# Kernel optimization log

Hardware: AMD Instinct MI355X
Metric: run time of the kernel (lower is better)

## Reference

```python
import jax, jax.numpy as jnp
import numpy as np

N = 20000      # tuple-graph nodes
E = 320000     # edges per relation
F_IN = 5189    # 80 one-hot + 3*1703 node features
DIM = 256
N_ORIG = 183   # original texas graph nodes
C = 7


def _gcn(x, W, b, src, dst, n):
    # PyG GCNConv: add self loops, symmetric deg^-1/2 normalization, aggregate src->dst.
    loop = jnp.arange(n)
    s = jnp.concatenate([src, loop])
    d = jnp.concatenate([dst, loop])
    deg = jax.ops.segment_sum(jnp.ones(s.shape[0], x.dtype), d, num_segments=n)
    dinv = jnp.where(deg > 0, jax.lax.rsqrt(deg), 0.0)
    norm = dinv[s] * dinv[d]            # [E+n]
    h = x @ W                            # [n, dim]
    out = jax.ops.segment_sum(h[s] * norm[:, None], d, num_segments=n)
    return out + b


def _mlp(h, w1, b1, w2, b2):
    return jnp.maximum(h @ w1 + b1, 0.0) @ w2 + b2


def _seg_mean(h, idx, n):
    s = jax.ops.segment_sum(h, idx, num_segments=n)
    cnt = jax.ops.segment_sum(jnp.ones(idx.shape[0], h.dtype), idx, num_segments=n)
    return s / jnp.maximum(cnt, 1.0)[:, None]


def setup_inputs() -> dict:
    key = jax.random.key(0)
    ks = jax.random.split(key, 16)
    sc_in = 1.0 / np.sqrt(F_IN)
    sc_d = 1.0 / np.sqrt(DIM)
    sc_3d = 1.0 / np.sqrt(3 * DIM)
    inp = {
        'x': jax.random.normal(ks[0], (N, F_IN), jnp.float32),
        'w1': jax.random.normal(ks[1], (3, F_IN, DIM), jnp.float32) * sc_in,
        'b1': jnp.zeros((3, DIM), jnp.float32),
        'w2': jax.random.normal(ks[2], (3, DIM, DIM), jnp.float32) * sc_d,
        'b2': jnp.zeros((3, DIM), jnp.float32),
        'm1w1': jax.random.normal(ks[3], (3 * DIM, DIM), jnp.float32) * sc_3d,
        'm1b1': jnp.zeros((DIM,), jnp.float32),
        'm1w2': jax.random.normal(ks[4], (DIM, DIM), jnp.float32) * sc_d,
        'm1b2': jnp.zeros((DIM,), jnp.float32),
        'm2w1': jax.random.normal(ks[5], (3 * DIM, DIM), jnp.float32) * sc_3d,
        'm2b1': jnp.zeros((DIM,), jnp.float32),
        'm2w2': jax.random.normal(ks[6], (DIM, DIM), jnp.float32) * sc_d,
        'm2b2': jnp.zeros((DIM,), jnp.float32),
        'mw1': jax.random.normal(ks[7], (3 * DIM, DIM), jnp.float32) * sc_3d,
        'mb1': jnp.zeros((DIM,), jnp.float32),
        'mw2': jax.random.normal(ks[8], (DIM, C), jnp.float32) * sc_d,
        'mb2': jnp.zeros((C,), jnp.float32),
        'edge_index_1': jax.random.randint(ks[9], (2, E), 0, N),
        'edge_index_2': jax.random.randint(ks[10], (2, E), 0, N),
        'edge_index_3': jax.random.randint(ks[11], (2, E), 0, N),
        'index_1': jax.random.randint(ks[12], (N,), 0, N_ORIG),
        'index_2': jax.random.randint(ks[13], (N,), 0, N_ORIG),
        'index_3': jax.random.randint(ks[14], (N,), 0, N_ORIG),
    }
    return inp


def reference(x, w1, b1, w2, b2, m1w1, m1b1, m1w2, m1b2,
              m2w1, m2b1, m2w2, m2b2, mw1, mb1, mw2, mb2,
              edge_index_1, edge_index_2, edge_index_3,
              index_1, index_2, index_3):
    n = x.shape[0]
    eis = (edge_index_1, edge_index_2, edge_index_3)
    # layer 1: three GCN convs over the three relations, ReLU, concat, MLP
    hs = [jnp.maximum(_gcn(x, w1[i], b1[i], eis[i][0], eis[i][1], n), 0.0) for i in range(3)]
    h = _mlp(jnp.concatenate(hs, axis=-1), m1w1, m1b1, m1w2, m1b2)
    # layer 2
    hs = [jnp.maximum(_gcn(h, w2[i], b2[i], eis[i][0], eis[i][1], n), 0.0) for i in range(3)]
    h = _mlp(jnp.concatenate(hs, axis=-1), m2w1, m2b1, m2w2, m2b2)
    # faithful to source bug: index_2 is overwritten by index_3 before scatter
    x1 = _seg_mean(h, index_1, N_ORIG)
    x2 = _seg_mean(h, index_3, N_ORIG)
    x3 = _seg_mean(h, index_3, N_ORIG)
    out = _mlp(jnp.concatenate([x1, x2, x3], axis=1), mw1, mb1, mw2, mb2)
    return jax.nn.log_softmax(out, axis=1)
```

## Files before the change

kernel.cpp:

```cpp
#include <hip/hip_runtime.h>
#include <hip/hip_bf16.h>
#include <cstdint>
#include <cstddef>

typedef __bf16 bf16_t;
typedef __bf16 bf16x8 __attribute__((ext_vector_type(8)));
typedef __bf16 bf16x4 __attribute__((ext_vector_type(4)));
typedef float f32x4 __attribute__((ext_vector_type(4)));

#define NN 20000
#define NE 320000
#define FIN 5189
#define KP1 5216
#define NORIG 183

__device__ inline f32x4 ld4u(const float* p) {
  f32x4 v; __builtin_memcpy(&v, p, 16); return v;
}

__device__ inline void gload_lds16(const bf16_t* g, bf16_t* l) {
  __builtin_amdgcn_global_load_lds(
      (const __attribute__((address_space(1))) uint32_t*)g,
      (__attribute__((address_space(3))) uint32_t*)l, 16, 0, 0);
}

__device__ inline int swz(int r) { return (r ^ (r >> 2)) & 3; }

__global__ void k_cvtpad(const float* __restrict__ x, bf16_t* __restrict__ xb) {
  const int total = NN * (KP1 / 8);
  for (int idx = blockIdx.x * 256 + threadIdx.x; idx < total; idx += gridDim.x * 256) {
    int row = idx / (KP1 / 8);
    int c8  = idx - row * (KP1 / 8);
    int col = c8 * 8;
    bf16x8 v{};
    const float* xp = x + (size_t)row * FIN + col;
    if (col + 8 <= FIN) {
      f32x4 a = ld4u(xp), b = ld4u(xp + 4);
#pragma unroll
      for (int j = 0; j < 4; ++j) { v[j] = (bf16_t)a[j]; v[4 + j] = (bf16_t)b[j]; }
    } else {
#pragma unroll
      for (int j = 0; j < 8; ++j) v[j] = (col + j < FIN) ? (bf16_t)xp[j] : (bf16_t)0.f;
    }
    *(bf16x8*)&xb[(size_t)row * KP1 + col] = v;
  }
}

__global__ __launch_bounds__(512) void k_gemm_w(
    const bf16_t* __restrict__ A, const bf16_t* __restrict__ Bt,
    bf16_t* __restrict__ C, const float* __restrict__ bias,
    const float* __restrict__ dscale,
    int M, int N, int Kp, int relu, int NBX)
{
  __shared__ __align__(16) bf16_t As[2][128 * 32];
  __shared__ __align__(16) bf16_t Bs[2][256 * 32];
  const int nwg = gridDim.x;
  const int q = nwg >> 3, rr = nwg & 7;
  const int xcd = blockIdx.x & 7, jj = blockIdx.x >> 3;
  const int L = (xcd < rr ? xcd * (q + 1) : rr * (q + 1) + (xcd - rr) * q) + jj;
  const int bx = L % NBX, by = L / NBX;

  const int tid = threadIdx.x, lane = tid & 63, wave = tid >> 6;
  const int m0 = by * 128, n0 = bx * 256;
  const int wr = (wave >> 2) * 64, wc = (wave & 3) * 64;
  const int fm = lane & 15, fs = lane >> 4;

  const int arow = tid >> 2, asl = tid & 3;
  const int aks = asl ^ swz(arow);
  int agrow = m0 + arow; if (agrow >= M) agrow = M - 1;
  const bf16_t* asrc = A + (size_t)agrow * Kp + aks * 8;

  const int br0 = tid >> 2, br1 = 128 + br0;
  const bf16_t* bsrc0 = Bt + (size_t)(n0 + br0) * Kp + (asl ^ swz(br0)) * 8;
  const bf16_t* bsrc1 = Bt + (size_t)(n0 + br1) * Kp + (asl ^ swz(br1)) * 8;

  bf16_t* adst  = &As[0][0] + wave * 512;
  bf16_t* bdst0 = &Bs[0][0] + wave * 512;
  bf16_t* bdst1 = &Bs[0][0] + 4096 + wave * 512;

  int aoff[4], boff[4];
#pragma unroll
  for (int i = 0; i < 4; ++i) {
    int ra = wr + i * 16 + fm;
    aoff[i] = ra * 32 + (fs ^ swz(ra)) * 8;
    int rb = wc + i * 16 + fm;
    boff[i] = rb * 32 + (fs ^ swz(rb)) * 8;
  }

  f32x4 acc[4][4];
#pragma unroll
  for (int i = 0; i < 4; ++i)
#pragma unroll
    for (int j = 0; j < 4; ++j) acc[i][j] = {0.f, 0.f, 0.f, 0.f};

#define STAGEW(buf, kof) do { \
    gload_lds16(asrc + (kof),  adst  + (buf) * (128 * 32)); \
    gload_lds16(bsrc0 + (kof), bdst0 + (buf) * (256 * 32)); \
    gload_lds16(bsrc1 + (kof), bdst1 + (buf) * (256 * 32)); \
  } while (0)

  const int NT = Kp / 32;
  STAGEW(0, 0);
  __syncthreads();
  int buf = 0;
  for (int t = 0; t < NT - 1; ++t) {
    STAGEW(buf ^ 1, (t + 1) * 32);
    bf16x8 af[4], bfv[4];
#pragma unroll
    for (int i = 0; i < 4; ++i) af[i] = *(const bf16x8*)&As[buf][aoff[i]];
#pragma unroll
    for (int j = 0; j < 4; ++j) bfv[j] = *(const bf16x8*)&Bs[buf][boff[j]];
#pragma unroll
    for (int i = 0; i < 4; ++i)
#pragma unroll
      for (int j = 0; j < 4; ++j)
        acc[i][j] = __builtin_amdgcn_mfma_f32_16x16x32_bf16(af[i], bfv[j], acc[i][j], 0, 0, 0);
    __syncthreads();
    buf ^= 1;
  }
  {
    bf16x8 af[4], bfv[4];
#pragma unroll
    for (int i = 0; i < 4; ++i) af[i] = *(const bf16x8*)&As[buf][aoff[i]];
#pragma unroll
    for (int j = 0; j < 4; ++j) bfv[j] = *(const bf16x8*)&Bs[buf][boff[j]];
#pragma unroll
    for (int i = 0; i < 4; ++i)
#pragma unroll
      for (int j = 0; j < 4; ++j)
        acc[i][j] = __builtin_amdgcn_mfma_f32_16x16x32_bf16(af[i], bfv[j], acc[i][j], 0, 0, 0);
  }

  const int ccol = n0 + wc + fm;
  const int rrel = (n0 + wc) >> 8;
  const float* dsp = dscale ? dscale + (size_t)rrel * NN : nullptr;
#pragma unroll
  for (int i = 0; i < 4; ++i) {
    const int rb2 = m0 + wr + i * 16 + (lane >> 4) * 4;
#pragma unroll
    for (int r = 0; r < 4; ++r) {
      const int row = rb2 + r;
      if (row < M) {
        bf16_t* cp = C + (size_t)row * N + ccol;
        const float sc = dsp ? dsp[row] : 1.f;
#pragma unroll
        for (int j = 0; j < 4; ++j) {
          float v = acc[i][j][r];
          if (bias) v += bias[ccol + j * 16];
          if (relu) v = fmaxf(v, 0.f);
          cp[j * 16] = (bf16_t)(v * sc);
        }
      }
    }
  }
}

__global__ __launch_bounds__(256) void k_gemm_s(
    const bf16_t* __restrict__ A, const bf16_t* __restrict__ Bt,
    bf16_t* __restrict__ C, const float* __restrict__ bias,
    int M, int N, int Kp, int relu)
{
  __shared__ __align__(16) bf16_t As[2][128 * 32];
  __shared__ __align__(16) bf16_t Bs[2][128 * 32];
  const int tid = threadIdx.x, lane = tid & 63, wave = tid >> 6;
  const int m0 = blockIdx.y * 128, n0 = blockIdx.x * 128;
  const int wr = (wave >> 1) * 64, wc = (wave & 1) * 64;
  const int fm = lane & 15, fs = lane >> 4;

  const int r0 = tid >> 2, r1 = 64 + r0, sl = tid & 3;
  int ag0 = m0 + r0; if (ag0 >= M) ag0 = M - 1;
  int ag1 = m0 + r1; if (ag1 >= M) ag1 = M - 1;
  const bf16_t* asrc0 = A + (size_t)ag0 * Kp + (sl ^ swz(r0)) * 8;
  const bf16_t* asrc1 = A + (size_t)ag1 * Kp + (sl ^ swz(r1)) * 8;
  const bf16_t* bsrc0 = Bt + (size_t)(n0 + r0) * Kp + (sl ^ swz(r0)) * 8;
  const bf16_t* bsrc1 = Bt + (size_t)(n0 + r1) * Kp + (sl ^ swz(r1)) * 8;

  bf16_t* adst0 = &As[0][0] + wave * 512;
  bf16_t* adst1 = &As[0][0] + 2048 + wave * 512;
  bf16_t* bdst0 = &Bs[0][0] + wave * 512;
  bf16_t* bdst1 = &Bs[0][0] + 2048 + wave * 512;

  int aoff[4], boff[4];
#pragma unroll
  for (int i = 0; i < 4; ++i) {
    int ra = wr + i * 16 + fm;
    aoff[i] = ra * 32 + (fs ^ swz(ra)) * 8;
    int rb = wc + i * 16 + fm;
    boff[i] = rb * 32 + (fs ^ swz(rb)) * 8;
  }

  f32x4 acc[4][4];
#pragma unroll
  for (int i = 0; i < 4; ++i)
#pragma unroll
    for (int j = 0; j < 4; ++j) acc[i][j] = {0.f, 0.f, 0.f, 0.f};

#define STAGES(buf, kof) do { \
    gload_lds16(asrc0 + (kof), adst0 + (buf) * (128 * 32)); \
    gload_lds16(asrc1 + (kof), adst1 + (buf) * (128 * 32)); \
    gload_lds16(bsrc0 + (kof), bdst0 + (buf) * (128 * 32)); \
    gload_lds16(bsrc1 + (kof), bdst1 + (buf) * (128 * 32)); \
  } while (0)

  const int NT = Kp / 32;
  STAGES(0, 0);
  __syncthreads();
  int buf = 0;
  for (int t = 0; t < NT - 1; ++t) {
    STAGES(buf ^ 1, (t + 1) * 32);
    bf16x8 af[4], bfv[4];
#pragma unroll
    for (int i = 0; i < 4; ++i) af[i] = *(const bf16x8*)&As[buf][aoff[i]];
#pragma unroll
    for (int j = 0; j < 4; ++j) bfv[j] = *(const bf16x8*)&Bs[buf][boff[j]];
#pragma unroll
    for (int i = 0; i < 4; ++i)
#pragma unroll
      for (int j = 0; j < 4; ++j)
        acc[i][j] = __builtin_amdgcn_mfma_f32_16x16x32_bf16(af[i], bfv[j], acc[i][j], 0, 0, 0);
    __syncthreads();
    buf ^= 1;
  }
  {
    bf16x8 af[4], bfv[4];
#pragma unroll
    for (int i = 0; i < 4; ++i) af[i] = *(const bf16x8*)&As[buf][aoff[i]];
#pragma unroll
    for (int j = 0; j < 4; ++j) bfv[j] = *(const bf16x8*)&Bs[buf][boff[j]];
#pragma unroll
    for (int i = 0; i < 4; ++i)
#pragma unroll
      for (int j = 0; j < 4; ++j)
        acc[i][j] = __builtin_amdgcn_mfma_f32_16x16x32_bf16(af[i], bfv[j], acc[i][j], 0, 0, 0);
  }

  const int ccol = n0 + wc + fm;
#pragma unroll
  for (int i = 0; i < 4; ++i) {
    const int rb2 = m0 + wr + i * 16 + (lane >> 4) * 4;
#pragma unroll
    for (int r = 0; r < 4; ++r) {
      const int row = rb2 + r;
      if (row < M) {
        bf16_t* cp = C + (size_t)row * N + ccol;
#pragma unroll
        for (int j = 0; j < 4; ++j) {
          float v = acc[i][j][r];
          if (bias) v += bias[ccol + j * 16];
          if (relu) v = fmaxf(v, 0.f);
          cp[j * 16] = (bf16_t)v;
        }
      }
    }
  }
}

__global__ void k_transw(const float* __restrict__ src, bf16_t* __restrict__ dst,
                         int K, int Kp)
{
  __shared__ float tile[32][33];
  const int g = blockIdx.z;
  const int k0 = blockIdx.x * 32, j0 = blockIdx.y * 32;
  const int tx = threadIdx.x, ty = threadIdx.y;
  const float* sp = src + (size_t)g * K * 256;
#pragma unroll
  for (int i = 0; i < 4; ++i) {
    int k = k0 + ty + i * 8;
    tile[ty + i * 8][tx] = (k < K) ? sp[(size_t)k * 256 + j0 + tx] : 0.f;
  }
  __syncthreads();
  bf16_t* dp = dst + (size_t)g * 256 * Kp;
#pragma unroll
  for (int i = 0; i < 4; ++i) {
    int n = j0 + ty + i * 8;
    dp[(size_t)n * Kp + k0 + tx] = (bf16_t)tile[tx][ty + i * 8];
  }
}

__global__ void k_deg3(const int* __restrict__ e1, const int* __restrict__ e2,
                       const int* __restrict__ e3, int* __restrict__ deg) {
  int i = blockIdx.x * 256 + threadIdx.x;
  if (i >= 3 * NE) return;
  int r = i / NE, e = i - r * NE;
  const int* d = (r == 0 ? e1 : (r == 1 ? e2 : e3)) + NE;
  atomicAdd(&deg[r * NN + d[e]], 1);
}

__global__ void k_degi(const int* __restrict__ i1, const int* __restrict__ i3,
                       int* __restrict__ deg183) {
  int i = blockIdx.x * 256 + threadIdx.x;
  if (i >= 2 * NN) return;
  int r = i / NN, v = i - r * NN;
  int g = (r ? i3 : i1)[v];
  atomicAdd(&deg183[r * NORIG + g], 1);
}

__global__ void k_dinv(const int* __restrict__ deg, float* __restrict__ dinv) {
  int v = blockIdx.x * 256 + threadIdx.x;
  if (v < 3 * NN) dinv[v] = rsqrtf((float)(deg[v] + 1));
}

#define SCAN_T 1024
#define SCAN_CH 20
__global__ __launch_bounds__(SCAN_T) void k_scan(
    const int* __restrict__ deg, int* __restrict__ rp, int* __restrict__ cur)
{
  const int r = blockIdx.x;
  const int* d = deg + r * NN;
  int* rpr = rp + r * (NN + 1);
  int* cr  = cur + r * NN;
  __shared__ int ts[SCAN_T];
  const int t = threadIdx.x;
  const int base = t * SCAN_CH;
  int local[SCAN_CH];
  int sum = 0;
#pragma unroll
  for (int i = 0; i < SCAN_CH; ++i) {
    int v = base + i;
    int x = (v < NN) ? d[v] : 0;
    local[i] = sum; sum += x;
  }
  ts[t] = sum; __syncthreads();
  for (int ofs = 1; ofs < SCAN_T; ofs <<= 1) {
    int v = ts[t];
    int w = (t >= ofs) ? ts[t - ofs] : 0;
    __syncthreads();
    ts[t] = v + w;
    __syncthreads();
  }
  int excl = (t == 0) ? 0 : ts[t - 1];
#pragma unroll
  for (int i = 0; i < SCAN_CH; ++i) {
    int v = base + i;
    if (v < NN) { int val = excl + local[i]; rpr[v] = val; cr[v] = val; }
  }
  if (t == SCAN_T - 1) rpr[NN] = ts[SCAN_T - 1];
}

__global__ void k_scan183(const int* __restrict__ deg183, int* __restrict__ rpg,
                          int* __restrict__ cur183) {
  const int r = blockIdx.x;
  const int* d = deg183 + r * NORIG;
  int* rpr = rpg + r * (NORIG + 1);
  int* cr  = cur183 + r * NORIG;
  __shared__ int ts[256];
  const int t = threadIdx.x;
  int x = (t < NORIG) ? d[t] : 0;
  ts[t] = x; __syncthreads();
  for (int o = 1; o < 256; o <<= 1) {
    int v = ts[t];
    int w = (t >= o) ? ts[t - o] : 0;
    __syncthreads();
    ts[t] = v + w;
    __syncthreads();
  }
  if (t < NORIG) {
    int excl = ts[t] - x;
    rpr[t] = excl; cr[t] = excl;
    if (t == NORIG - 1) rpr[NORIG] = ts[t];
  }
}

__global__ void k_bucket3(const int* __restrict__ e1, const int* __restrict__ e2,
                          const int* __restrict__ e3, int* __restrict__ cur,
                          int* __restrict__ col) {
  int i = blockIdx.x * 256 + threadIdx.x;
  if (i >= 3 * NE) return;
  int r = i / NE, e = i - r * NE;
  const int* ei = (r == 0 ? e1 : (r == 1 ? e2 : e3));
  int d = ei[NE + e];
  int pos = atomicAdd(&cur[r * NN + d], 1);
  col[(size_t)r * NE + pos] = ei[e];
}

__global__ void k_bucketi(const int* __restrict__ i1, const int* __restrict__ i3,
                          int* __restrict__ cur183, int* __restrict__ colg) {
  int i = blockIdx.x * 256 + threadIdx.x;
  if (i >= 2 * NN) return;
  int r = i / NN, v = i - r * NN;
  int g = (r ? i3 : i1)[v];
  int pos = atomicAdd(&cur183[r * NORIG + g], 1);
  colg[r * NN + pos] = v;
}

__global__ __launch_bounds__(256) void k_gatherb(
    const bf16_t* __restrict__ P, bf16_t* __restrict__ Out,
    const int* __restrict__ rp, const int* __restrict__ col,
    const float* __restrict__ dinv, const float* __restrict__ bias)
{
  const int wv = threadIdx.x >> 6, lane = threadIdx.x & 63;
  const int v = blockIdx.x * 4 + wv;
  const int r = blockIdx.y;
  const int roff = r << 8;
  const int* rpr = rp + r * (NN + 1);
  const int* cr  = col + (size_t)r * NE;
  const float dv = dinv[r * NN + v];
  const int c0 = roff + lane * 4;

  bf16x4 hs = *(const bf16x4*)&P[(size_t)v * 768 + c0];
  float a0 = (float)hs[0], a1 = (float)hs[1], a2 = (float)hs[2], a3 = (float)hs[3];

  int i = rpr[v];
  const int e = rpr[v + 1];
  for (; i + 8 <= e; i += 8) {
    bf16x4 h[8];
#pragma unroll
    for (int u = 0; u < 8; ++u) {
      int s = cr[i + u];
      h[u] = *(const bf16x4*)&P[(size_t)s * 768 + c0];
    }
#pragma unroll
    for (int u = 0; u < 8; ++u) {
      a0 += (float)h[u][0]; a1 += (float)h[u][1];
      a2 += (float)h[u][2]; a3 += (float)h[u][3];
    }
  }
  for (; i < e; ++i) {
    int s = cr[i];
    bf16x4 h = *(const bf16x4*)&P[(size_t)s * 768 + c0];
    a0 += (float)h[0]; a1 += (float)h[1];
    a2 += (float)h[2]; a3 += (float)h[3];
  }
  f32x4 bb = ld4u(bias + c0);
  bf16x4 o;
  o[0] = (bf16_t)fmaxf(dv * a0 + bb[0], 0.f);
  o[1] = (bf16_t)fmaxf(dv * a1 + bb[1], 0.f);
  o[2] = (bf16_t)fmaxf(dv * a2 + bb[2], 0.f);
  o[3] = (bf16_t)fmaxf(dv * a3 + bb[3], 0.f);
  *(bf16x4*)&Out[(size_t)v * 768 + c0] = o;
}

__global__ __launch_bounds__(256) void k_final2(
    const bf16_t* __restrict__ h2,
    const int* __restrict__ rpg, const int* __restrict__ colg,
    const float* __restrict__ mw1, const float* __restrict__ mb1,
    const float* __restrict__ mw2, const float* __restrict__ mb2,
    float* __restrict__ out)
{
  __shared__ float xc[768];
  __shared__ float tt[256];
  __shared__ float lg[8];
  const int g = blockIdx.x, tid = threadIdx.x;
  const int* rp1 = rpg;
  const int* rp3 = rpg + (NORIG + 1);
  const int* c1v = colg;
  const int* c3v = colg + NN;

  float a1 = 0.f;
  int b1 = rp1[g], e1 = rp1[g + 1];
  for (int i = b1; i < e1; ++i) a1 += (float)h2[(size_t)c1v[i] * 256 + tid];
  float a3 = 0.f;
  int b3 = rp3[g], e3 = rp3[g + 1];
  for (int i = b3; i < e3; ++i) a3 += (float)h2[(size_t)c3v[i] * 256 + tid];
  a1 *= 1.f / fmaxf((float)(e1 - b1), 1.f);
  a3 *= 1.f / fmaxf((float)(e3 - b3), 1.f);
  xc[tid] = a1;
  xc[256 + tid] = a3;
  xc[512 + tid] = a3;
  __syncthreads();
  float acc = mb1[tid];
  for (int k = 0; k < 768; ++k) acc += xc[k] * mw1[k * 256 + tid];
  tt[tid] = fmaxf(acc, 0.f);
  __syncthreads();
  if (tid < 7) {
    float a = mb2[tid];
    for (int k = 0; k < 256; ++k) a += tt[k] * mw2[k * 7 + tid];
    lg[tid] = a;
  }
  __syncthreads();
  if (tid == 0) {
    float mx = lg[0];
    for (int c2 = 1; c2 < 7; ++c2) mx = fmaxf(mx, lg[c2]);
    float sum = 0.f;
    for (int c2 = 0; c2 < 7; ++c2) sum += expf(lg[c2] - mx);
    float lse = logf(sum) + mx;
    for (int c2 = 0; c2 < 7; ++c2) out[g * 7 + c2] = lg[c2] - lse;
  }
}

extern "C" void kernel_launch(void* const* d_in, const int* in_sizes, int n_in,
                              void* d_out, int out_size, void* d_ws, size_t ws_size,
                              hipStream_t stream) {
  const float* x    = (const float*)d_in[0];
  const float* w1   = (const float*)d_in[1];
  const float* b1   = (const float*)d_in[2];
  const float* w2   = (const float*)d_in[3];
  const float* b2   = (const float*)d_in[4];
  const float* m1w1 = (const float*)d_in[5];
  const float* m1b1 = (const float*)d_in[6];
  const float* m1w2 = (const float*)d_in[7];
  const float* m1b2 = (const float*)d_in[8];
  const float* m2w1 = (const float*)d_in[9];
  const float* m2b1 = (const float*)d_in[10];
  const float* m2w2 = (const float*)d_in[11];
  const float* m2b2 = (const float*)d_in[12];
  const float* mw1  = (const float*)d_in[13];
  const float* mb1  = (const float*)d_in[14];
  const float* mw2  = (const float*)d_in[15];
  const float* mb2  = (const float*)d_in[16];
  const int* e1 = (const int*)d_in[17];
  const int* e2 = (const int*)d_in[18];
  const int* e3 = (const int*)d_in[19];
  const int* i1 = (const int*)d_in[20];
  const int* i3 = (const int*)d_in[22];
  float* out = (float*)d_out;

  char* ws = (char*)d_ws;
  size_t off = 0;
  auto alloc = [&](size_t bytes) {
    char* p = ws + off;
    off += (bytes + 255) & ~(size_t)255;
    return (void*)p;
  };
  bf16_t* xb   = (bf16_t*)alloc((size_t)NN * KP1 * 2);
  bf16_t* wt   = (bf16_t*)alloc((size_t)768 * KP1 * 2);
  bf16_t* a1   = (bf16_t*)alloc((size_t)NN * 768 * 2);
  bf16_t* g1   = (bf16_t*)alloc((size_t)NN * 768 * 2);
  bf16_t* t1   = (bf16_t*)alloc((size_t)NN * 256 * 2);
  bf16_t* h1   = (bf16_t*)alloc((size_t)NN * 256 * 2);
  int*    deg  = (int*)alloc(((size_t)3 * NN + 2 * NORIG) * 4);
  float*  dinv = (float*)alloc((size_t)3 * NN * 4);
  int*    rp   = (int*)alloc((size_t)3 * (NN + 1) * 4);
  int*    cur  = (int*)alloc((size_t)3 * NN * 4);
  int*    col  = (int*)alloc((size_t)3 * NE * 4);
  int*    rpg  = (int*)alloc((size_t)2 * (NORIG + 1) * 4);
  int*    cur183 = (int*)alloc((size_t)2 * NORIG * 4);
  int*    colg = (int*)alloc((size_t)2 * NN * 4);
  int*    deg183 = deg + 3 * NN;

  hipMemsetAsync(deg, 0, ((size_t)3 * NN + 2 * NORIG) * 4, stream);
  k_deg3<<<(3 * NE + 255) / 256, 256, 0, stream>>>(e1, e2, e3, deg);
  k_degi<<<(2 * NN + 255) / 256, 256, 0, stream>>>(i1, i3, deg183);
  k_dinv<<<(3 * NN + 255) / 256, 256, 0, stream>>>(deg, dinv);
  k_scan<<<3, SCAN_T, 0, stream>>>(deg, rp, cur);
  k_scan183<<<2, 256, 0, stream>>>(deg183, rpg, cur183);
  k_bucket3<<<(3 * NE + 255) / 256, 256, 0, stream>>>(e1, e2, e3, cur, col);
  k_bucketi<<<(2 * NN + 255) / 256, 256, 0, stream>>>(i1, i3, cur183, colg);

  auto transw = [&](const float* Wsrc, int G, int K, int Kp) {
    k_transw<<<dim3(Kp / 32, 8, G), dim3(32, 8), 0, stream>>>(Wsrc, wt, K, Kp);
  };

  dim3 ggat(NN / 4, 3);
  const int NWGW = 3 * 157;

  transw(w1, 3, FIN, KP1);
  k_cvtpad<<<2048, 256, 0, stream>>>(x, xb);
  k_gemm_w<<<NWGW, 512, 0, stream>>>(xb, wt, a1, nullptr, dinv, NN, 768, KP1, 0, 3);
  k_gatherb<<<ggat, 256, 0, stream>>>(a1, g1, rp, col, dinv, b1);
  transw(m1w1, 1, 768, 768);
  k_gemm_s<<<dim3(2, 157), 256, 0, stream>>>(g1, wt, t1, m1b1, NN, 256, 768, 1);
  transw(m1w2, 1, 256, 256);
  k_gemm_s<<<dim3(2, 157), 256, 0, stream>>>(t1, wt, h1, m1b2, NN, 256, 256, 0);

  transw(w2, 3, 256, 256);
  k_gemm_w<<<NWGW, 512, 0, stream>>>(h1, wt, a1, nullptr, dinv, NN, 768, 256, 0, 3);
  k_gatherb<<<ggat, 256, 0, stream>>>(a1, g1, rp, col, dinv, b2);
  transw(m2w1, 1, 768, 768);
  k_gemm_s<<<dim3(2, 157), 256, 0, stream>>>(g1, wt, t1, m2b1, NN, 256, 768, 1);
  transw(m2w2, 1, 256, 256);
  k_gemm_s<<<dim3(2, 157), 256, 0, stream>>>(t1, wt, h1, m2b2, NN, 256, 256, 0);

  k_final2<<<NORIG, 256, 0, stream>>>(h1, rpg, colg, mw1, mb1, mw2, mb2, out);
}
```

Measured before the change: 874.1 us.

## Unify GEMMs into one 128x128-tile kernel with XCD remap and deeper gather unroll

```diff
diff --git a/kernel.cpp b/kernel.cpp
--- a/kernel.cpp
+++ b/kernel.cpp
@@ -46,14 +46,14 @@
   }
 }
 
-__global__ __launch_bounds__(512) void k_gemm_w(
+__global__ __launch_bounds__(256) void k_gemm_s(
     const bf16_t* __restrict__ A, const bf16_t* __restrict__ Bt,
     bf16_t* __restrict__ C, const float* __restrict__ bias,
     const float* __restrict__ dscale,
     int M, int N, int Kp, int relu, int NBX)
 {
   __shared__ __align__(16) bf16_t As[2][128 * 32];
-  __shared__ __align__(16) bf16_t Bs[2][256 * 32];
+  __shared__ __align__(16) bf16_t Bs[2][128 * 32];
   const int nwg = gridDim.x;
   const int q = nwg >> 3, rr = nwg & 7;
   const int xcd = blockIdx.x & 7, jj = blockIdx.x >> 3;
@@ -61,109 +61,7 @@
   const int bx = L % NBX, by = L / NBX;
 
   const int tid = threadIdx.x, lane = tid & 63, wave = tid >> 6;
-  const int m0 = by * 128, n0 = bx * 256;
-  const int wr = (wave >> 2) * 64, wc = (wave & 3) * 64;
-  const int fm = lane & 15, fs = lane >> 4;
-
-  const int arow = tid >> 2, asl = tid & 3;
-  const int aks = asl ^ swz(arow);
-  int agrow = m0 + arow; if (agrow >= M) agrow = M - 1;
-  const bf16_t* asrc = A + (size_t)agrow * Kp + aks * 8;
-
-  const int br0 = tid >> 2, br1 = 128 + br0;
-  const bf16_t* bsrc0 = Bt + (size_t)(n0 + br0) * Kp + (asl ^ swz(br0)) * 8;
-  const bf16_t* bsrc1 = Bt + (size_t)(n0 + br1) * Kp + (asl ^ swz(br1)) * 8;
-
-  bf16_t* adst  = &As[0][0] + wave * 512;
-  bf16_t* bdst0 = &Bs[0][0] + wave * 512;
-  bf16_t* bdst1 = &Bs[0][0] + 4096 + wave * 512;
-
-  int aoff[4], boff[4];
-#pragma unroll
-  for (int i = 0; i < 4; ++i) {
-    int ra = wr + i * 16 + fm;
-    aoff[i] = ra * 32 + (fs ^ swz(ra)) * 8;
-    int rb = wc + i * 16 + fm;
-    boff[i] = rb * 32 + (fs ^ swz(rb)) * 8;
-  }
-
-  f32x4 acc[4][4];
-#pragma unroll
-  for (int i = 0; i < 4; ++i)
-#pragma unroll
-    for (int j = 0; j < 4; ++j) acc[i][j] = {0.f, 0.f, 0.f, 0.f};
-
-#define STAGEW(buf, kof) do { \
-    gload_lds16(asrc + (kof),  adst  + (buf) * (128 * 32)); \
-    gload_lds16(bsrc0 + (kof), bdst0 + (buf) * (256 * 32)); \
-    gload_lds16(bsrc1 + (kof), bdst1 + (buf) * (256 * 32)); \
-  } while (0)
-
-  const int NT = Kp / 32;
-  STAGEW(0, 0);
-  __syncthreads();
-  int buf = 0;
-  for (int t = 0; t < NT - 1; ++t) {
-    STAGEW(buf ^ 1, (t + 1) * 32);
-    bf16x8 af[4], bfv[4];
-#pragma unroll
-    for (int i = 0; i < 4; ++i) af[i] = *(const bf16x8*)&As[buf][aoff[i]];
-#pragma unroll
-    for (int j = 0; j < 4; ++j) bfv[j] = *(const bf16x8*)&Bs[buf][boff[j]];
-#pragma unroll
-    for (int i = 0; i < 4; ++i)
-#pragma unroll
-      for (int j = 0; j < 4; ++j)
-        acc[i][j] = __builtin_amdgcn_mfma_f32_16x16x32_bf16(af[i], bfv[j], acc[i][j], 0, 0, 0);
-    __syncthreads();
-    buf ^= 1;
-  }
-  {
-    bf16x8 af[4], bfv[4];
-#pragma unroll
-    for (int i = 0; i < 4; ++i) af[i] = *(const bf16x8*)&As[buf][aoff[i]];
-#pragma unroll
-    for (int j = 0; j < 4; ++j) bfv[j] = *(const bf16x8*)&Bs[buf][boff[j]];
-#pragma unroll
-    for (int i = 0; i < 4; ++i)
-#pragma unroll
-      for (int j = 0; j < 4; ++j)
-        acc[i][j] = __builtin_amdgcn_mfma_f32_16x16x32_bf16(af[i], bfv[j], acc[i][j], 0, 0, 0);
-  }
-
-  const int ccol = n0 + wc + fm;
-  const int rrel = (n0 + wc) >> 8;
-  const float* dsp = dscale ? dscale + (size_t)rrel * NN : nullptr;
-#pragma unroll
-  for (int i = 0; i < 4; ++i) {
-    const int rb2 = m0 + wr + i * 16 + (lane >> 4) * 4;
-#pragma unroll
-    for (int r = 0; r < 4; ++r) {
-      const int row = rb2 + r;
-      if (row < M) {
-        bf16_t* cp = C + (size_t)row * N + ccol;
-        const float sc = dsp ? dsp[row] : 1.f;
-#pragma unroll
-        for (int j = 0; j < 4; ++j) {
-          float v = acc[i][j][r];
-          if (bias) v += bias[ccol + j * 16];
-          if (relu) v = fmaxf(v, 0.f);
-          cp[j * 16] = (bf16_t)(v * sc);
-        }
-      }
-    }
-  }
-}
-
-__global__ __launch_bounds__(256) void k_gemm_s(
-    const bf16_t* __restrict__ A, const bf16_t* __restrict__ Bt,
-    bf16_t* __restrict__ C, const float* __restrict__ bias,
-    int M, int N, int Kp, int relu)
-{
-  __shared__ __align__(16) bf16_t As[2][128 * 32];
-  __shared__ __align__(16) bf16_t Bs[2][128 * 32];
-  const int tid = threadIdx.x, lane = tid & 63, wave = tid >> 6;
-  const int m0 = blockIdx.y * 128, n0 = blockIdx.x * 128;
+  const int m0 = by * 128, n0 = bx * 128;
   const int wr = (wave >> 1) * 64, wc = (wave & 1) * 64;
   const int fm = lane & 15, fs = lane >> 4;
 
@@ -235,6 +133,8 @@
   }
 
   const int ccol = n0 + wc + fm;
+  const int rrel = (n0 + wc) >> 8;
+  const float* dsp = dscale ? dscale + (size_t)rrel * NN : nullptr;
 #pragma unroll
   for (int i = 0; i < 4; ++i) {
     const int rb2 = m0 + wr + i * 16 + (lane >> 4) * 4;
@@ -243,12 +143,13 @@
       const int row = rb2 + r;
       if (row < M) {
         bf16_t* cp = C + (size_t)row * N + ccol;
+        const float sc = dsp ? dsp[row] : 1.f;
 #pragma unroll
         for (int j = 0; j < 4; ++j) {
           float v = acc[i][j][r];
           if (bias) v += bias[ccol + j * 16];
           if (relu) v = fmaxf(v, 0.f);
-          cp[j * 16] = (bf16_t)v;
+          cp[j * 16] = (bf16_t)(v * sc);
         }
       }
     }
@@ -402,15 +303,28 @@
 
   int i = rpr[v];
   const int e = rpr[v + 1];
-  for (; i + 8 <= e; i += 8) {
-    bf16x4 h[8];
-#pragma unroll
-    for (int u = 0; u < 8; ++u) {
+  for (; i + 16 <= e; i += 16) {
+    bf16x4 h[16];
+#pragma unroll
+    for (int u = 0; u < 16; ++u) {
       int s = cr[i + u];
       h[u] = *(const bf16x4*)&P[(size_t)s * 768 + c0];
     }
 #pragma unroll
-    for (int u = 0; u < 8; ++u) {
+    for (int u = 0; u < 16; ++u) {
+      a0 += (float)h[u][0]; a1 += (float)h[u][1];
+      a2 += (float)h[u][2]; a3 += (float)h[u][3];
+    }
+  }
+  for (; i + 4 <= e; i += 4) {
+    bf16x4 h[4];
+#pragma unroll
+    for (int u = 0; u < 4; ++u) {
+      int s = cr[i + u];
+      h[u] = *(const bf16x4*)&P[(size_t)s * 768 + c0];
+    }
+#pragma unroll
+    for (int u = 0; u < 4; ++u) {
       a0 += (float)h[u][0]; a1 += (float)h[u][1];
       a2 += (float)h[u][2]; a3 += (float)h[u][3];
     }
@@ -542,24 +456,25 @@
   };
 
   dim3 ggat(NN / 4, 3);
-  const int NWGW = 3 * 157;
+  const int G768 = 6 * 157;
+  const int G256 = 2 * 157;
 
   transw(w1, 3, FIN, KP1);
   k_cvtpad<<<2048, 256, 0, stream>>>(x, xb);
-  k_gemm_w<<<NWGW, 512, 0, stream>>>(xb, wt, a1, nullptr, dinv, NN, 768, KP1, 0, 3);
+  k_gemm_s<<<G768, 256, 0, stream>>>(xb, wt, a1, nullptr, dinv, NN, 768, KP1, 0, 6);
   k_gatherb<<<ggat, 256, 0, stream>>>(a1, g1, rp, col, dinv, b1);
   transw(m1w1, 1, 768, 768);
-  k_gemm_s<<<dim3(2, 157), 256, 0, stream>>>(g1, wt, t1, m1b1, NN, 256, 768, 1);
+  k_gemm_s<<<G256, 256, 0, stream>>>(g1, wt, t1, m1b1, nullptr, NN, 256, 768, 1, 2);
   transw(m1w2, 1, 256, 256);
-  k_gemm_s<<<dim3(2, 157), 256, 0, stream>>>(t1, wt, h1, m1b2, NN, 256, 256, 0);
+  k_gemm_s<<<G256, 256, 0, stream>>>(t1, wt, h1, m1b2, nullptr, NN, 256, 256, 0, 2);
 
   transw(w2, 3, 256, 256);
-  k_gemm_w<<<NWGW, 512, 0, stream>>>(h1, wt, a1, nullptr, dinv, NN, 768, 256, 0, 3);
+  k_gemm_s<<<G768, 256, 0, stream>>>(h1, wt, a1, nullptr, dinv, NN, 768, 256, 0, 6);
   k_gatherb<<<ggat, 256, 0, stream>>>(a1, g1, rp, col, dinv, b2);
   transw(m2w1, 1, 768, 768);
-  k_gemm_s<<<dim3(2, 157), 256, 0, stream>>>(g1, wt, t1, m2b1, NN, 256, 768, 1);
+  k_gemm_s<<<G256, 256, 0, stream>>>(g1, wt, t1, m2b1, nullptr, NN, 256, 768, 1, 2);
   transw(m2w2, 1, 256, 256);
-  k_gemm_s<<<dim3(2, 157), 256, 0, stream>>>(t1, wt, h1, m2b2, NN, 256, 256, 0);
+  k_gemm_s<<<G256, 256, 0, stream>>>(t1, wt, h1, m2b2, nullptr, NN, 256, 256, 0, 2);
 
   k_final2<<<NORIG, 256, 0, stream>>>(h1, rpg, colg, mw1, mb1, mw2, mb2, out);
 }
```

Result: slower. 1.020 ms (+16.6%).
